# Optimization experiments

Hardware: AMD Instinct MI355X
Metric: run time of the kernel (lower is better)

Reference implementation:

```python
import jax, jax.numpy as jnp
import numpy as np

B, K, PS, DP = 8, 8, 128, 16           # batch, patches/example, patch px, dino patch size
D, NH, HD, L = 1024, 8, 128, 2         # embed dim, heads, head dim, transformer layers
GRID = PS // DP                        # 8 tokens per side
TPP = GRID * GRID                      # 64 tokens per patch


def _conv(x, w, stride, pad):
    return jax.lax.conv_general_dilated(x, w, (stride, stride), pad,
                                        dimension_numbers=('NCHW', 'OIHW', 'NCHW'))


def _ln(x, g, b, eps=1e-5):
    m = jnp.mean(x, -1, keepdims=True)
    v = jnp.var(x, -1, keepdims=True)
    return (x - m) * jax.lax.rsqrt(v + eps) * g + b


def _bn(x, g, b, m, v, eps=1e-5):
    inv = jax.lax.rsqrt(v + eps)
    return (x - m[:, None, None]) * inv[:, None, None] * g[:, None, None] + b[:, None, None]


def _up2(x):  # bilinear x2, align_corners=False (half-pixel, matches jax.image.resize)
    n, c, h, w = x.shape
    return jax.image.resize(x, (n, c, 2 * h, 2 * w), method='linear')


def _mha(x, wqkv, bqkv, wo, bo):
    b, s, d = x.shape
    qkv = x @ wqkv.T + bqkv
    q, k, v = jnp.split(qkv, 3, axis=-1)
    q = q.reshape(b, s, NH, HD).transpose(0, 2, 1, 3)
    k = k.reshape(b, s, NH, HD).transpose(0, 2, 1, 3)
    v = v.reshape(b, s, NH, HD).transpose(0, 2, 1, 3)
    att = jax.nn.softmax(jnp.einsum('bhqd,bhkd->bhqk', q, k) / jnp.sqrt(jnp.float32(HD)), axis=-1)
    o = jnp.einsum('bhqk,bhkd->bhqd', att, v).transpose(0, 2, 1, 3).reshape(b, s, d)
    return o @ wo.T + bo


def setup_inputs() -> dict:
    key = jax.random.key(0)
    ks = iter(jax.random.split(key, 40))

    def rn(shape, s=0.02):
        return jax.random.normal(next(ks), shape, jnp.float32) * s

    inp = {}
    inp['patches'] = jax.random.normal(next(ks), (B, K, 3, PS, PS), jnp.float32)
    inp['pe_w'] = rn((D, 3, DP, DP))
    inp['pe_b'] = jnp.zeros((D,), jnp.float32)
    inp['qkv_w'] = rn((L, 3 * D, D))
    inp['qkv_b'] = jnp.zeros((L, 3 * D), jnp.float32)
    inp['out_w'] = rn((L, D, D))
    inp['out_b'] = jnp.zeros((L, D), jnp.float32)
    inp['ln1_g'] = jnp.ones((L, D), jnp.float32)
    inp['ln1_b'] = jnp.zeros((L, D), jnp.float32)
    inp['ff1_w'] = rn((L, 4 * D, D))
    inp['ff1_b'] = jnp.zeros((L, 4 * D), jnp.float32)
    inp['ff2_w'] = rn((L, D, 4 * D))
    inp['ff2_b'] = jnp.zeros((L, D), jnp.float32)
    inp['ln2_g'] = jnp.ones((L, D), jnp.float32)
    inp['ln2_b'] = jnp.zeros((L, D), jnp.float32)
    chans = [(512, D), (256, 512), (128, 256), (64, 128)]
    for i, (co, ci) in enumerate(chans, 1):
        inp[f'dw{i}'] = rn((co, ci, 3, 3), 0.05)
        inp[f'db{i}'] = jnp.zeros((co,), jnp.float32)
        inp[f'g{i}'] = jnp.ones((co,), jnp.float32)
        inp[f'be{i}'] = jnp.zeros((co,), jnp.float32)
        inp[f'm{i}'] = jnp.zeros((co,), jnp.float32)
        inp[f'v{i}'] = jnp.ones((co,), jnp.float32)
    inp['dw5'] = rn((1, 64, 1, 1), 0.05)
    inp['db5'] = jnp.zeros((1,), jnp.float32)
    return inp


def reference(patches, pe_w, pe_b, qkv_w, qkv_b, out_w, out_b, ln1_g, ln1_b,
              ff1_w, ff1_b, ff2_w, ff2_b, ln2_g, ln2_b,
              dw1, db1, g1, be1, m1, v1, dw2, db2, g2, be2, m2, v2,
              dw3, db3, g3, be3, m3, v3, dw4, db4, g4, be4, m4, v4, dw5, db5):
    b, k = patches.shape[:2]
    x = patches.reshape(b * k, 3, PS, PS)
    # frozen DINO patch embedding (runs under torch.no_grad in the original)
    hs = _conv(x, pe_w, DP, 'VALID') + pe_b[None, :, None, None]     # [BK, D, GRID, GRID]
    hs = jax.lax.stop_gradient(hs)
    hs = hs.reshape(b * k, D, TPP).transpose(0, 2, 1).reshape(b, k * TPP, D)
    # post-norm TransformerEncoder (norm_first=False, gelu), dropout=eval (identity)
    for i in range(L):
        hs = _ln(hs + _mha(hs, qkv_w[i], qkv_b[i], out_w[i], out_b[i]), ln1_g[i], ln1_b[i])
        ff = jax.nn.gelu(hs @ ff1_w[i].T + ff1_b[i], approximate=False) @ ff2_w[i].T + ff2_b[i]
        hs = _ln(hs + ff, ln2_g[i], ln2_b[i])
    fm = hs.reshape(b * k, TPP, D).transpose(0, 2, 1).reshape(b * k, D, GRID, GRID)
    # CNN decoder: (conv3x3 -> BN(eval) -> ReLU -> bilinear x2) x4 -> conv1x1
    y = _up2(jax.nn.relu(_bn(_conv(fm, dw1, 1, 'SAME') + db1[None, :, None, None], g1, be1, m1, v1)))
    y = _up2(jax.nn.relu(_bn(_conv(y, dw2, 1, 'SAME') + db2[None, :, None, None], g2, be2, m2, v2)))
    y = _up2(jax.nn.relu(_bn(_conv(y, dw3, 1, 'SAME') + db3[None, :, None, None], g3, be3, m3, v3)))
    y = _up2(jax.nn.relu(_bn(_conv(y, dw4, 1, 'SAME') + db4[None, :, None, None], g4, be4, m4, v4)))
    y = _conv(y, dw5, 1, 'VALID') + db5[None, :, None, None]          # [BK, 1, PS, PS]
    return y.reshape(b, k, 1, PS, PS)
```

## Files before the change

### kernel.cpp

```cpp
#include <hip/hip_runtime.h>
#include <stdint.h>


typedef unsigned short u16;
typedef __bf16 bf16x8 __attribute__((ext_vector_type(8)));
typedef short  s16x8  __attribute__((ext_vector_type(8)));
typedef float  f32x4  __attribute__((ext_vector_type(4)));

__device__ __forceinline__ float b2f(u16 x) { return __uint_as_float(((unsigned)x) << 16); }
__device__ __forceinline__ u16 f2b(float f) {
  unsigned u = __float_as_uint(f);
  unsigned r = (u + 0x7fffu + ((u >> 16) & 1u)) >> 16;
  return (u16)r;
}
__device__ __forceinline__ void async16(u16* lds, const u16* g) {
  __builtin_amdgcn_global_load_lds((const __attribute__((address_space(1))) void*)g,
                                   (__attribute__((address_space(3))) void*)lds, 16, 0, 0);
}
__device__ __forceinline__ float gelu_f(float x) {
  return 0.5f * x * (1.0f + erff(x * 0.70710678118654752f));
}

__global__ __launch_bounds__(256) void cvt_f2b(const float* __restrict__ src,
                                               u16* __restrict__ dst, int n) {
  const int i = (blockIdx.x * 256 + threadIdx.x) * 4;
  if (i + 3 < n) {
    const float4 v = *(const float4*)(src + i);
    dst[i] = f2b(v.x); dst[i + 1] = f2b(v.y); dst[i + 2] = f2b(v.z); dst[i + 3] = f2b(v.w);
  }
}

__global__ __launch_bounds__(256) void gemm_bt(
    const u16* __restrict__ A, int lda, long long sAb, long long sAh,
    const u16* __restrict__ B, int ldb, long long sBb, long long sBh,
    u16* __restrict__ Cb, int ldc, long long sCb, long long sCh,
    const float* __restrict__ bias, int epi, int ZH, int nk)
{
  __shared__ u16 As[3][128 * 32];
  __shared__ u16 Bs[3][128 * 32];
  const int tid = threadIdx.x;
  const int zb = blockIdx.z / ZH, zh = blockIdx.z % ZH;
  const u16* Ab = A + zb * sAb + zh * sAh;
  const u16* Bb = B + zb * sBb + zh * sBh;
  const int m0 = blockIdx.y << 7, n0 = blockIdx.x << 7;
  const int wave = tid >> 6, lane = tid & 63;
  const int wm = (wave >> 1) << 6, wn = (wave & 1) << 6;
  const int lr = lane & 15, lq = lane >> 4;
  const int rowb = tid >> 2;
  const int kc_e = (((tid & 3) ^ ((tid >> 3) & 3)) << 3);
  const int kslot = ((lq ^ ((lr >> 1) & 3)) << 3);

  const u16* Arow0 = Ab + (long long)(m0 + rowb)      * lda + kc_e;
  const u16* Arow1 = Ab + (long long)(m0 + rowb + 64) * lda + kc_e;
  const u16* Brow0 = Bb + (long long)(n0 + rowb)      * ldb + kc_e;
  const u16* Brow1 = Bb + (long long)(n0 + rowb + 64) * ldb + kc_e;

  f32x4 acc[4][4] = {};

  auto stage = [&](int kt, int b) {
    const int k0 = kt << 5;
    async16(&As[b][tid * 8],         Arow0 + k0);
    async16(&As[b][(tid + 256) * 8], Arow1 + k0);
    async16(&Bs[b][tid * 8],         Brow0 + k0);
    async16(&Bs[b][(tid + 256) * 8], Brow1 + k0);
  };

  stage(0, 0);
  if (nk > 1) stage(1, 1);
  int cur = 0;
  for (int kt = 0; kt < nk; ++kt) {
    if (kt + 2 < nk) {
      int nb = cur + 2; if (nb >= 3) nb -= 3;
      stage(kt + 2, nb);
      asm volatile("s_waitcnt vmcnt(8)" ::: "memory");
    } else if (kt + 1 < nk) {
      asm volatile("s_waitcnt vmcnt(4)" ::: "memory");
    } else {
      asm volatile("s_waitcnt vmcnt(0)" ::: "memory");
    }
    asm volatile("s_barrier" ::: "memory");

    bf16x8 af[4], bfv[4];
#pragma unroll
    for (int mi = 0; mi < 4; ++mi)
      af[mi] = __builtin_bit_cast(bf16x8, *(const s16x8*)&As[cur][((wm + mi * 16 + lr) << 5) + kslot]);
#pragma unroll
    for (int ni = 0; ni < 4; ++ni)
      bfv[ni] = __builtin_bit_cast(bf16x8, *(const s16x8*)&Bs[cur][((wn + ni * 16 + lr) << 5) + kslot]);
#pragma unroll
    for (int mi = 0; mi < 4; ++mi)
#pragma unroll
      for (int ni = 0; ni < 4; ++ni)
        acc[mi][ni] = __builtin_amdgcn_mfma_f32_16x16x32_bf16(af[mi], bfv[ni], acc[mi][ni], 0, 0, 0);

    asm volatile("s_barrier" ::: "memory");
    ++cur; if (cur == 3) cur = 0;
  }

  const long long Co = zb * sCb + zh * sCh;
#pragma unroll
  for (int ni = 0; ni < 4; ++ni) {
    const int col = n0 + wn + ni * 16 + lr;
    const float badd = bias ? bias[col] : 0.0f;
#pragma unroll
    for (int mi = 0; mi < 4; ++mi) {
      const int row0 = m0 + wm + mi * 16 + (lq << 2);
#pragma unroll
      for (int r = 0; r < 4; ++r) {
        float v = acc[mi][ni][r] + badd;
        if (epi == 1) v = gelu_f(v);
        Cb[Co + (long long)(row0 + r) * ldc + col] = f2b(v);
      }
    }
  }
}

__global__ __launch_bounds__(256) void conv_gemm(
    const u16* __restrict__ U, const u16* __restrict__ Wr,
    u16* __restrict__ Out,
    const float* __restrict__ bn_g, const float* __restrict__ bn_b,
    const float* __restrict__ bn_m, const float* __restrict__ bn_v,
    const float* __restrict__ cb,
    const u16* __restrict__ zpg,
    int H, int W, int l2w, int l2hw, int l2c, int CoutReal, int Kdim, int nk)
{
  __shared__ u16 As[3][128 * 32];
  __shared__ u16 Bs[3][64 * 32];
  const int tid = threadIdx.x;
  const int m0 = blockIdx.x << 7, n0 = blockIdx.y << 6;
  const int wave = tid >> 6, lane = tid & 63;
  const int wm = (wave >> 1) << 6, wn = (wave & 1) << 5;
  const int lr = lane & 15, lq = lane >> 4;
  const int rowb = tid >> 2;
  const int kc_e = (((tid & 3) ^ ((tid >> 3) & 3)) << 3);
  const int kslot = ((lq ^ ((lr >> 1) & 3)) << 3);
  const int hwmask = (1 << l2hw) - 1, wmask = (1 << l2w) - 1, cmask = (1 << l2c) - 1;

  int yA[2], xA[2];
  long long baseA[2];
  {
#pragma unroll
    for (int i = 0; i < 2; ++i) {
      const int mrow = m0 + rowb + (i << 6);
      const int img = mrow >> l2hw;
      const int rem = mrow & hwmask;
      yA[i] = rem >> l2w; xA[i] = rem & wmask;
      baseA[i] = (long long)(img << l2hw);
    }
  }
  const u16* Bbase = Wr + (long long)(n0 + rowb) * Kdim + kc_e;

  f32x4 acc[4][2] = {};

  auto stage = [&](int kt, int b) {
    const int k0 = kt << 5;
    const int k = k0 + kc_e;
    const int t = k >> l2c, ci = k & cmask;
    const int dy = (t * 86) >> 8;
    const int dx = t - dy * 3;
#pragma unroll
    for (int i = 0; i < 2; ++i) {
      const int yy = yA[i] + dy - 1, xx = xA[i] + dx - 1;
      const u16* src = ((unsigned)yy < (unsigned)H && (unsigned)xx < (unsigned)W)
          ? U + (((baseA[i] + (yy << l2w) + xx) << l2c) + ci)
          : zpg;
      async16(&As[b][(tid + (i << 8)) * 8], src);
    }
    async16(&Bs[b][tid * 8], Bbase + k0);
  };

  stage(0, 0);
  stage(1, 1);

  for (int t0 = 0; t0 < nk; t0 += 3) {
#pragma unroll
    for (int p = 0; p < 3; ++p) {
      const int tt = t0 + p;
      if (tt + 2 < nk) {
        stage(tt + 2, (p + 2) % 3);
        asm volatile("s_waitcnt vmcnt(6)" ::: "memory");
      } else if (tt + 1 < nk) {
        asm volatile("s_waitcnt vmcnt(3)" ::: "memory");
      } else {
        asm volatile("s_waitcnt vmcnt(0)" ::: "memory");
      }
      asm volatile("s_barrier" ::: "memory");

      bf16x8 af[4], bfv[2];
#pragma unroll
      for (int mi = 0; mi < 4; ++mi)
        af[mi] = __builtin_bit_cast(bf16x8, *(const s16x8*)&As[p][((wm + mi * 16 + lr) << 5) + kslot]);
#pragma unroll
      for (int ni = 0; ni < 2; ++ni)
        bfv[ni] = __builtin_bit_cast(bf16x8, *(const s16x8*)&Bs[p][((wn + ni * 16 + lr) << 5) + kslot]);
#pragma unroll
      for (int mi = 0; mi < 4; ++mi)
#pragma unroll
        for (int ni = 0; ni < 2; ++ni)
          acc[mi][ni] = __builtin_amdgcn_mfma_f32_16x16x32_bf16(af[mi], bfv[ni], acc[mi][ni], 0, 0, 0);

      asm volatile("s_barrier" ::: "memory");
    }
  }

#pragma unroll
  for (int ni = 0; ni < 2; ++ni) {
    const int col = n0 + wn + ni * 16 + lr;
    const bool ok = col < CoutReal;
    float bs = 0.0f, bsh = 0.0f;
    if (ok) {
      const float inv = rsqrtf(bn_v[col] + 1e-5f);
      bs = bn_g[col] * inv;
      bsh = (cb[col] - bn_m[col]) * bs + bn_b[col];
    }
#pragma unroll
    for (int mi = 0; mi < 4; ++mi) {
      const int row0 = m0 + wm + mi * 16 + (lq << 2);
#pragma unroll
      for (int r = 0; r < 4; ++r) {
        if (ok) {
          const float v = fmaxf(acc[mi][ni][r] * bs + bsh, 0.0f);
          Out[(long long)(row0 + r) * CoutReal + col] = f2b(v);
        }
      }
    }
  }
}


__global__ void pe_gather(const float* __restrict__ patches, u16* __restrict__ Ape) {
  const int t = blockIdx.x, tid = threadIdx.x;
  const int img = t >> 6, pos = t & 63, ty = pos >> 3, tx = pos & 7;
  const float* base = patches + (long long)img * 3 * 128 * 128;
  u16* dst = Ape + (long long)t * 768;
  for (int k = tid; k < 768; k += 256) {
    const int c = k >> 8, rr = k & 255, ky = rr >> 4, kx = rr & 15;
    dst[k] = f2b(base[c * 16384 + (ty * 16 + ky) * 128 + tx * 16 + kx]);
  }
}

__global__ void vt_transpose(const u16* __restrict__ qkv, u16* __restrict__ Vt) {
  __shared__ u16 lds[64 * 130];
  const int tt = blockIdx.x;
  const int z = blockIdx.y;
  const int bq = z >> 3, h = z & 7;
  const int tid = threadIdx.x;
  for (int idx = tid; idx < 64 * 128; idx += 256) {
    const int t = idx >> 7, d = idx & 127;
    lds[t * 130 + d] = qkv[(long long)(bq * 512 + tt * 64 + t) * 3072 + 2048 + h * 128 + d];
  }
  __syncthreads();
  for (int idx = tid; idx < 64 * 128; idx += 256) {
    const int d = idx >> 6, t = idx & 63;
    Vt[(long long)z * 65536 + d * 512 + tt * 64 + t] = lds[t * 130 + d];
  }
}

__global__ __launch_bounds__(256) void softmax_rows(u16* __restrict__ P) {
  __shared__ float red[8];
  const long long base = (long long)blockIdx.x * 512;
  const int tid = threadIdx.x;
  const float sc = 0.08838834764831845f;
  float x0 = b2f(P[base + tid]) * sc;
  float x1 = b2f(P[base + tid + 256]) * sc;
  float mx = fmaxf(x0, x1);
  for (int o = 32; o; o >>= 1) mx = fmaxf(mx, __shfl_down(mx, o));
  if ((tid & 63) == 0) red[tid >> 6] = mx;
  __syncthreads();
  mx = fmaxf(fmaxf(red[0], red[1]), fmaxf(red[2], red[3]));
  const float e0 = expf(x0 - mx), e1 = expf(x1 - mx);
  float s = e0 + e1;
  for (int o = 32; o; o >>= 1) s += __shfl_down(s, o);
  __syncthreads();
  if ((tid & 63) == 0) red[tid >> 6] = s;
  __syncthreads();
  s = red[0] + red[1] + red[2] + red[3];
  const float inv = 1.0f / s;
  P[base + tid] = f2b(e0 * inv);
  P[base + tid + 256] = f2b(e1 * inv);
}

__global__ __launch_bounds__(256) void ln_kernel(
    u16* __restrict__ hsb, const u16* __restrict__ P,
    const float* __restrict__ gw, const float* __restrict__ bw)
{
  __shared__ float red[8];
  const int r = blockIdx.x, tid = threadIdx.x;
  float x[4], s = 0.0f, s2 = 0.0f;
#pragma unroll
  for (int i = 0; i < 4; ++i) {
    const int c = tid + i * 256;
    const float v = b2f(hsb[(long long)r * 1024 + c]) + b2f(P[(long long)r * 1024 + c]);
    x[i] = v; s += v; s2 += v * v;
  }
  for (int o = 32; o; o >>= 1) { s += __shfl_down(s, o); s2 += __shfl_down(s2, o); }
  if ((tid & 63) == 0) { red[tid >> 6] = s; red[4 + (tid >> 6)] = s2; }
  __syncthreads();
  s  = red[0] + red[1] + red[2] + red[3];
  s2 = red[4] + red[5] + red[6] + red[7];
  const float mean = s * (1.0f / 1024.0f);
  const float var = s2 * (1.0f / 1024.0f) - mean * mean;
  const float inv = rsqrtf(var + 1e-5f);
#pragma unroll
  for (int i = 0; i < 4; ++i) {
    const int c = tid + i * 256;
    const float y = (x[i] - mean) * inv * gw[c] + bw[c];
    hsb[(long long)r * 1024 + c] = f2b(y);
  }
}

__global__ void repack_w(const float* __restrict__ src, u16* __restrict__ dst, int Cout, int l2c) {
  const int co = blockIdx.x, tid = threadIdx.x;
  const int Cin = 1 << l2c, K9 = 9 << l2c;
  for (int j = tid; j < K9; j += 256) {
    const int t = j >> l2c, ci = j & (Cin - 1);
    u16 v = 0;
    if (co < Cout) v = f2b(src[(long long)(co * Cin + ci) * 9 + t]);
    dst[(long long)co * K9 + j] = v;
  }
}

__global__ void ups2x(const u16* __restrict__ in, u16* __restrict__ out,
                      int l2h, int l2w, int l2c, long long total)
{
  const long long idx = (long long)blockIdx.x * 256 + threadIdx.x;
  if (idx >= total) return;
  const int H = 1 << l2h, W = 1 << l2w, C = 1 << l2c;
  const int c = (int)(idx & (C - 1));
  long long t = idx >> l2c;
  const int ox = (int)(t & (2 * W - 1)); t >>= (l2w + 1);
  const int oy = (int)(t & (2 * H - 1)); t >>= (l2h + 1);
  const int img = (int)t;
  const int iy = oy >> 1, ix = ox >> 1;
  int y0, y1, x0, x1; float wy0, wy1, wx0, wx1;
  if (oy & 1) { y0 = iy; y1 = min(iy + 1, H - 1); wy0 = 0.75f; wy1 = 0.25f; }
  else        { y0 = max(iy - 1, 0); y1 = iy;     wy0 = 0.25f; wy1 = 0.75f; }
  if (ox & 1) { x0 = ix; x1 = min(ix + 1, W - 1); wx0 = 0.75f; wx1 = 0.25f; }
  else        { x0 = max(ix - 1, 0); x1 = ix;     wx0 = 0.25f; wx1 = 0.75f; }
  const u16* base = in + (((long long)img) << (l2h + l2w + l2c));
  const float v00 = b2f(base[((((long long)y0 << l2w) + x0) << l2c) + c]);
  const float v01 = b2f(base[((((long long)y0 << l2w) + x1) << l2c) + c]);
  const float v10 = b2f(base[((((long long)y1 << l2w) + x0) << l2c) + c]);
  const float v11 = b2f(base[((((long long)y1 << l2w) + x1) << l2c) + c]);
  out[idx] = f2b(wy0 * (wx0 * v00 + wx1 * v01) + wy1 * (wx0 * v10 + wx1 * v11));
}

__global__ __launch_bounds__(256) void conv1x1_final(
    const u16* __restrict__ C4, const float* __restrict__ w5,
    const float* __restrict__ b5, float* __restrict__ Z)
{
  const int tid = threadIdx.x;
  const int px = blockIdx.x * 4 + (tid >> 6);
  const int lane = tid & 63;
  float v = b2f(C4[(long long)px * 64 + lane]) * w5[lane];
  for (int o = 32; o; o >>= 1) v += __shfl_down(v, o);
  if (lane == 0) Z[px] = v + b5[0];
}

__global__ void ups_final(const float* __restrict__ Z, float* __restrict__ out) {
  const int idx = blockIdx.x * 256 + threadIdx.x;
  const int ox = idx & 127, oy = (idx >> 7) & 127, img = idx >> 14;
  const int iy = oy >> 1, ix = ox >> 1;
  int y0, y1, x0, x1; float wy0, wy1, wx0, wx1;
  if (oy & 1) { y0 = iy; y1 = min(iy + 1, 63); wy0 = 0.75f; wy1 = 0.25f; }
  else        { y0 = max(iy - 1, 0); y1 = iy;  wy0 = 0.25f; wy1 = 0.75f; }
  if (ox & 1) { x0 = ix; x1 = min(ix + 1, 63); wx0 = 0.75f; wx1 = 0.25f; }
  else        { x0 = max(ix - 1, 0); x1 = ix;  wx0 = 0.25f; wx1 = 0.75f; }
  const float* zi = Z + (long long)img * 4096;
  const float v = wy0 * (wx0 * zi[y0 * 64 + x0] + wx1 * zi[y0 * 64 + x1]) +
                  wy1 * (wx0 * zi[y1 * 64 + x0] + wx1 * zi[y1 * 64 + x1]);
  out[idx] = v;
}

extern "C" void kernel_launch(void* const* d_in, const int* in_sizes, int n_in,
                              void* d_out, int out_size, void* d_ws, size_t ws_size,
                              hipStream_t stream)
{
  (void)in_sizes; (void)n_in; (void)out_size;
  if (ws_size < 110395648u) return;
  const float* patches = (const float*)d_in[0];
  const float* pe_w = (const float*)d_in[1];
  const float* pe_b = (const float*)d_in[2];
  const float* qkv_w = (const float*)d_in[3];
  const float* qkv_b = (const float*)d_in[4];
  const float* out_w = (const float*)d_in[5];
  const float* out_b = (const float*)d_in[6];
  const float* ln1_g = (const float*)d_in[7];
  const float* ln1_b = (const float*)d_in[8];
  const float* ff1_w = (const float*)d_in[9];
  const float* ff1_b = (const float*)d_in[10];
  const float* ff2_w = (const float*)d_in[11];
  const float* ff2_b = (const float*)d_in[12];
  const float* ln2_g = (const float*)d_in[13];
  const float* ln2_b = (const float*)d_in[14];
  const float* dwv[4] = {(const float*)d_in[15], (const float*)d_in[21], (const float*)d_in[27], (const float*)d_in[33]};
  const float* dbv[4] = {(const float*)d_in[16], (const float*)d_in[22], (const float*)d_in[28], (const float*)d_in[34]};
  const float* gv[4]  = {(const float*)d_in[17], (const float*)d_in[23], (const float*)d_in[29], (const float*)d_in[35]};
  const float* bev[4] = {(const float*)d_in[18], (const float*)d_in[24], (const float*)d_in[30], (const float*)d_in[36]};
  const float* mv[4]  = {(const float*)d_in[19], (const float*)d_in[25], (const float*)d_in[31], (const float*)d_in[37]};
  const float* vv[4]  = {(const float*)d_in[20], (const float*)d_in[26], (const float*)d_in[32], (const float*)d_in[38]};
  const float* dw5 = (const float*)d_in[39];
  const float* db5 = (const float*)d_in[40];
  float* outp = (float*)d_out;
  char* ws = (char*)d_ws;

  u16* HS_B = (u16*)(ws + 0);
  u16* APE  = (u16*)(ws + 8388608);
  u16* QKV  = (u16*)(ws + 8388608);
  u16* VT   = (u16*)(ws + 33554432);
  u16* SF   = (u16*)(ws + 41943040);
  u16* FF1G = (u16*)(ws + 41943040);
  u16* ATT  = (u16*)(ws + 75497472);
  u16* P_B  = (u16*)(ws + 83886080);
  u16* W1   = (u16*)(ws + 92274688);
  u16* W2   = (u16*)(ws + 100663296);
  u16* WR1 = (u16*)(ws + 8388608);
  u16* WR2 = (u16*)(ws + 17825792);
  u16* WR3 = (u16*)(ws + 20185088);
  u16* C1  = (u16*)(ws + 20774912);
  u16* U1  = (u16*)(ws + 24969216);
  u16* C2  = (u16*)(ws + 41746432);
  u16* U2  = (u16*)(ws + 50135040);
  u16* C3  = (u16*)(ws + 83689472);
  u16* U3  = (u16*)(ws + 8388608);
  u16* C4  = (u16*)(ws + 75497472);
  u16* ZPG = (u16*)(ws + 109051904);
  u16* WR4 = (u16*)(ws + 109052160);
  float* Z = (float*)(ws + 109347072);

  pe_gather<<<4096, 256, 0, stream>>>(patches, APE);
  cvt_f2b<<<768, 256, 0, stream>>>(pe_w, W1, 786432);
  gemm_bt<<<dim3(8, 32, 1), 256, 0, stream>>>(
      APE, 768, 0, 0, W1, 768, 0, 0,
      HS_B, 1024, 0, 0, pe_b, 0, 1, 24);

  for (int l = 0; l < 2; ++l) {
    cvt_f2b<<<3072, 256, 0, stream>>>(qkv_w + (long long)l * 3145728, W1, 3145728);
    gemm_bt<<<dim3(24, 32, 1), 256, 0, stream>>>(
        HS_B, 1024, 0, 0, W1, 1024, 0, 0,
        QKV, 3072, 0, 0, qkv_b + l * 3072, 0, 1, 32);
    vt_transpose<<<dim3(8, 64), 256, 0, stream>>>(QKV, VT);
    gemm_bt<<<dim3(4, 4, 64), 256, 0, stream>>>(
        QKV, 3072, 1572864, 128, QKV + 1024, 3072, 1572864, 128,
        SF, 512, 2097152, 262144, nullptr, 0, 8, 4);
    softmax_rows<<<32768, 256, 0, stream>>>(SF);
    gemm_bt<<<dim3(1, 4, 64), 256, 0, stream>>>(
        SF, 512, 2097152, 262144, VT, 512, 524288, 65536,
        ATT, 1024, 524288, 128, nullptr, 0, 8, 16);
    cvt_f2b<<<1024, 256, 0, stream>>>(out_w + (long long)l * 1048576, W2, 1048576);
    gemm_bt<<<dim3(8, 32, 1), 256, 0, stream>>>(
        ATT, 1024, 0, 0, W2, 1024, 0, 0,
        P_B, 1024, 0, 0, out_b + l * 1024, 0, 1, 32);
    ln_kernel<<<4096, 256, 0, stream>>>(HS_B, P_B, ln1_g + l * 1024, ln1_b + l * 1024);
    cvt_f2b<<<4096, 256, 0, stream>>>(ff1_w + (long long)l * 4194304, W1, 4194304);
    cvt_f2b<<<4096, 256, 0, stream>>>(ff2_w + (long long)l * 4194304, W2, 4194304);
    gemm_bt<<<dim3(32, 32, 1), 256, 0, stream>>>(
        HS_B, 1024, 0, 0, W1, 1024, 0, 0,
        FF1G, 4096, 0, 0, ff1_b + l * 4096, 1, 1, 32);
    gemm_bt<<<dim3(8, 32, 1), 256, 0, stream>>>(
        FF1G, 4096, 0, 0, W2, 4096, 0, 0,
        P_B, 1024, 0, 0, ff2_b + l * 1024, 0, 1, 128);
    ln_kernel<<<4096, 256, 0, stream>>>(HS_B, P_B, ln2_g + l * 1024, ln2_b + l * 1024);
  }

  hipMemsetAsync((void*)ZPG, 0, 256, stream);
  repack_w<<<512, 256, 0, stream>>>(dwv[0], WR1, 512, 10);
  repack_w<<<256, 256, 0, stream>>>(dwv[1], WR2, 256, 9);
  repack_w<<<128, 256, 0, stream>>>(dwv[2], WR3, 128, 8);
  repack_w<<<128, 256, 0, stream>>>(dwv[3], WR4, 64, 7);

  conv_gemm<<<dim3(32, 8, 1), 256, 0, stream>>>(
      HS_B, WR1, C1, gv[0], bev[0], mv[0], vv[0], dbv[0], ZPG,
      8, 8, 3, 6, 10, 512, 9216, 288);
  ups2x<<<32768, 256, 0, stream>>>(C1, U1, 3, 3, 9, 8388608LL);
  conv_gemm<<<dim3(128, 4, 1), 256, 0, stream>>>(
      U1, WR2, C2, gv[1], bev[1], mv[1], vv[1], dbv[1], ZPG,
      16, 16, 4, 8, 9, 256, 4608, 144);
  ups2x<<<65536, 256, 0, stream>>>(C2, U2, 4, 4, 8, 16777216LL);
  conv_gemm<<<dim3(512, 2, 1), 256, 0, stream>>>(
      U2, WR3, C3, gv[2], bev[2], mv[2], vv[2], dbv[2], ZPG,
      32, 32, 5, 10, 8, 128, 2304, 72);
  ups2x<<<131072, 256, 0, stream>>>(C3, U3, 5, 5, 7, 33554432LL);
  conv_gemm<<<dim3(2048, 1, 1), 256, 0, stream>>>(
      U3, WR4, C4, gv[3], bev[3], mv[3], vv[3], dbv[3], ZPG,
      64, 64, 6, 12, 7, 64, 1152, 36);
  conv1x1_final<<<65536, 256, 0, stream>>>(C4, dw5, db5, Z);
  ups_final<<<4096, 256, 0, stream>>>(Z, outp);
}
```

Measured before the change: 1.396 ms.

## Split-K low-occupancy GEMMs and early convs with fp32 partial reduction kernels

After: 1.306 ms. 6.5% less time.

```diff
diff --git a/kernel.cpp b/kernel.cpp
--- a/kernel.cpp
+++ b/kernel.cpp
@@ -34,7 +34,8 @@
     const u16* __restrict__ A, int lda, long long sAb, long long sAh,
     const u16* __restrict__ B, int ldb, long long sBb, long long sBh,
     u16* __restrict__ Cb, int ldc, long long sCb, long long sCh,
-    const float* __restrict__ bias, int epi, int ZH, int nk)
+    const float* __restrict__ bias, int epi, int ZH, int nk,
+    float* __restrict__ Part)
 {
   __shared__ u16 As[3][128 * 32];
   __shared__ u16 Bs[3][128 * 32];
@@ -47,13 +48,14 @@
   const int wm = (wave >> 1) << 6, wn = (wave & 1) << 6;
   const int lr = lane & 15, lq = lane >> 4;
   const int rowb = tid >> 2;
+  const int koff = Part ? (zb * (nk << 5)) : 0;
   const int kc_e = (((tid & 3) ^ ((tid >> 3) & 3)) << 3);
   const int kslot = ((lq ^ ((lr >> 1) & 3)) << 3);
 
-  const u16* Arow0 = Ab + (long long)(m0 + rowb)      * lda + kc_e;
-  const u16* Arow1 = Ab + (long long)(m0 + rowb + 64) * lda + kc_e;
-  const u16* Brow0 = Bb + (long long)(n0 + rowb)      * ldb + kc_e;
-  const u16* Brow1 = Bb + (long long)(n0 + rowb + 64) * ldb + kc_e;
+  const u16* Arow0 = Ab + (long long)(m0 + rowb)      * lda + kc_e + koff;
+  const u16* Arow1 = Ab + (long long)(m0 + rowb + 64) * lda + kc_e + koff;
+  const u16* Brow0 = Bb + (long long)(n0 + rowb)      * ldb + kc_e + koff;
+  const u16* Brow1 = Bb + (long long)(n0 + rowb + 64) * ldb + kc_e + koff;
 
   f32x4 acc[4][4] = {};
 
@@ -97,6 +99,22 @@
     ++cur; if (cur == 3) cur = 0;
   }
 
+  if (Part) {
+    float* P = Part + (long long)zb * sCb;
+#pragma unroll
+    for (int ni = 0; ni < 4; ++ni) {
+      const int col = n0 + wn + ni * 16 + lr;
+#pragma unroll
+      for (int mi = 0; mi < 4; ++mi) {
+        const int row0 = m0 + wm + mi * 16 + (lq << 2);
+#pragma unroll
+        for (int r = 0; r < 4; ++r)
+          P[(long long)(row0 + r) * ldc + col] = acc[mi][ni][r];
+      }
+    }
+    return;
+  }
+
   const long long Co = zb * sCb + zh * sCh;
 #pragma unroll
   for (int ni = 0; ni < 4; ++ni) {
@@ -112,6 +130,49 @@
         Cb[Co + (long long)(row0 + r) * ldc + col] = f2b(v);
       }
     }
+  }
+}
+
+__global__ __launch_bounds__(256) void reduce_bias(
+    const float* __restrict__ Part, long long sPart, int S,
+    const float* __restrict__ bias, int N,
+    u16* __restrict__ Out, long long total)
+{
+  const long long i = ((long long)blockIdx.x * 256 + threadIdx.x) * 4;
+  if (i >= total) return;
+  f32x4 s = *(const f32x4*)(Part + i);
+  for (int p = 1; p < S; ++p) {
+    const f32x4 v = *(const f32x4*)(Part + (long long)p * sPart + i);
+    s[0] += v[0]; s[1] += v[1]; s[2] += v[2]; s[3] += v[3];
+  }
+  const int colb = (int)(i & (N - 1));
+#pragma unroll
+  for (int j = 0; j < 4; ++j)
+    Out[i + j] = f2b(s[j] + bias[colb + j]);
+}
+
+__global__ __launch_bounds__(256) void reduce_bn(
+    const float* __restrict__ Part, long long sPart, int S,
+    const float* __restrict__ bn_g, const float* __restrict__ bn_b,
+    const float* __restrict__ bn_m, const float* __restrict__ bn_v,
+    const float* __restrict__ cb, int Cout,
+    u16* __restrict__ Out, long long total)
+{
+  const long long i = ((long long)blockIdx.x * 256 + threadIdx.x) * 4;
+  if (i >= total) return;
+  f32x4 s = *(const f32x4*)(Part + i);
+  for (int p = 1; p < S; ++p) {
+    const f32x4 v = *(const f32x4*)(Part + (long long)p * sPart + i);
+    s[0] += v[0]; s[1] += v[1]; s[2] += v[2]; s[3] += v[3];
+  }
+  const int colb = (int)(i & (Cout - 1));
+#pragma unroll
+  for (int j = 0; j < 4; ++j) {
+    const int col = colb + j;
+    const float inv = rsqrtf(bn_v[col] + 1e-5f);
+    const float bs = bn_g[col] * inv;
+    const float bsh = (cb[col] - bn_m[col]) * bs + bn_b[col];
+    Out[i + j] = f2b(fmaxf(s[j] * bs + bsh, 0.0f));
   }
 }
 
@@ -122,12 +183,15 @@
     const float* __restrict__ bn_m, const float* __restrict__ bn_v,
     const float* __restrict__ cb,
     const u16* __restrict__ zpg,
-    int H, int W, int l2w, int l2hw, int l2c, int CoutReal, int Kdim, int nk)
+    int H, int W, int l2w, int l2hw, int l2c, int CoutReal, int Kdim, int nk,
+    float* __restrict__ Part, long long sPart)
 {
   __shared__ u16 As[3][128 * 32];
   __shared__ u16 Bs[3][64 * 32];
   const int tid = threadIdx.x;
   const int m0 = blockIdx.x << 7, n0 = blockIdx.y << 6;
+  const int slice = blockIdx.z;
+  const int koff = Part ? (slice * (nk << 5)) : 0;
   const int wave = tid >> 6, lane = tid & 63;
   const int wm = (wave >> 1) << 6, wn = (wave & 1) << 5;
   const int lr = lane & 15, lq = lane >> 4;
@@ -148,14 +212,14 @@
       baseA[i] = (long long)(img << l2hw);
     }
   }
-  const u16* Bbase = Wr + (long long)(n0 + rowb) * Kdim + kc_e;
+  const u16* Bbase = Wr + (long long)(n0 + rowb) * Kdim + kc_e + koff;
 
   f32x4 acc[4][2] = {};
 
   auto stage = [&](int kt, int b) {
     const int k0 = kt << 5;
-    const int k = k0 + kc_e;
-    const int t = k >> l2c, ci = k & cmask;
+    const int kabs = koff + k0 + kc_e;
+    const int t = kabs >> l2c, ci = kabs & cmask;
     const int dy = (t * 86) >> 8;
     const int dx = t - dy * 3;
 #pragma unroll
@@ -201,6 +265,22 @@
 
       asm volatile("s_barrier" ::: "memory");
     }
+  }
+
+  if (Part) {
+    float* P = Part + (long long)slice * sPart;
+#pragma unroll
+    for (int ni = 0; ni < 2; ++ni) {
+      const int col = n0 + wn + ni * 16 + lr;
+#pragma unroll
+      for (int mi = 0; mi < 4; ++mi) {
+        const int row0 = m0 + wm + mi * 16 + (lq << 2);
+#pragma unroll
+        for (int r = 0; r < 4; ++r)
+          P[(long long)(row0 + r) * CoutReal + col] = acc[mi][ni][r];
+      }
+    }
+    return;
   }
 
 #pragma unroll
@@ -414,6 +494,8 @@
   u16* P_B  = (u16*)(ws + 83886080);
   u16* W1   = (u16*)(ws + 92274688);
   u16* W2   = (u16*)(ws + 100663296);
+  float* PART_G  = (float*)(ws + 8388608);
+  float* PART_PE = (float*)(ws + 41943040);
   u16* WR1 = (u16*)(ws + 8388608);
   u16* WR2 = (u16*)(ws + 17825792);
   u16* WR3 = (u16*)(ws + 20185088);
@@ -424,42 +506,47 @@
   u16* C3  = (u16*)(ws + 83689472);
   u16* U3  = (u16*)(ws + 8388608);
   u16* C4  = (u16*)(ws + 75497472);
+  float* PARTC1 = (float*)(ws + 41746432);
+  float* PARTC2 = (float*)(ws + 50331648);
   u16* ZPG = (u16*)(ws + 109051904);
   u16* WR4 = (u16*)(ws + 109052160);
   float* Z = (float*)(ws + 109347072);
 
   pe_gather<<<4096, 256, 0, stream>>>(patches, APE);
   cvt_f2b<<<768, 256, 0, stream>>>(pe_w, W1, 786432);
-  gemm_bt<<<dim3(8, 32, 1), 256, 0, stream>>>(
+  gemm_bt<<<dim3(8, 32, 2), 256, 0, stream>>>(
       APE, 768, 0, 0, W1, 768, 0, 0,
-      HS_B, 1024, 0, 0, pe_b, 0, 1, 24);
+      HS_B, 1024, 4194304, 0, nullptr, 0, 1, 12, PART_PE);
+  reduce_bias<<<4096, 256, 0, stream>>>(PART_PE, 4194304, 2, pe_b, 1024, HS_B, 4194304LL);
 
   for (int l = 0; l < 2; ++l) {
     cvt_f2b<<<3072, 256, 0, stream>>>(qkv_w + (long long)l * 3145728, W1, 3145728);
     gemm_bt<<<dim3(24, 32, 1), 256, 0, stream>>>(
         HS_B, 1024, 0, 0, W1, 1024, 0, 0,
-        QKV, 3072, 0, 0, qkv_b + l * 3072, 0, 1, 32);
+        QKV, 3072, 0, 0, qkv_b + l * 3072, 0, 1, 32, nullptr);
     vt_transpose<<<dim3(8, 64), 256, 0, stream>>>(QKV, VT);
     gemm_bt<<<dim3(4, 4, 64), 256, 0, stream>>>(
         QKV, 3072, 1572864, 128, QKV + 1024, 3072, 1572864, 128,
-        SF, 512, 2097152, 262144, nullptr, 0, 8, 4);
+        SF, 512, 2097152, 262144, nullptr, 0, 8, 4, nullptr);
     softmax_rows<<<32768, 256, 0, stream>>>(SF);
     gemm_bt<<<dim3(1, 4, 64), 256, 0, stream>>>(
         SF, 512, 2097152, 262144, VT, 512, 524288, 65536,
-        ATT, 1024, 524288, 128, nullptr, 0, 8, 16);
+        ATT, 1024, 524288, 128, nullptr, 0, 8, 16, nullptr);
     cvt_f2b<<<1024, 256, 0, stream>>>(out_w + (long long)l * 1048576, W2, 1048576);
-    gemm_bt<<<dim3(8, 32, 1), 256, 0, stream>>>(
+    gemm_bt<<<dim3(8, 32, 2), 256, 0, stream>>>(
         ATT, 1024, 0, 0, W2, 1024, 0, 0,
-        P_B, 1024, 0, 0, out_b + l * 1024, 0, 1, 32);
+        P_B, 1024, 4194304, 0, nullptr, 0, 1, 16, PART_G);
+    reduce_bias<<<4096, 256, 0, stream>>>(PART_G, 4194304, 2, out_b + l * 1024, 1024, P_B, 4194304LL);
     ln_kernel<<<4096, 256, 0, stream>>>(HS_B, P_B, ln1_g + l * 1024, ln1_b + l * 1024);
     cvt_f2b<<<4096, 256, 0, stream>>>(ff1_w + (long long)l * 4194304, W1, 4194304);
     cvt_f2b<<<4096, 256, 0, stream>>>(ff2_w + (long long)l * 4194304, W2, 4194304);
     gemm_bt<<<dim3(32, 32, 1), 256, 0, stream>>>(
         HS_B, 1024, 0, 0, W1, 1024, 0, 0,
-        FF1G, 4096, 0, 0, ff1_b + l * 4096, 1, 1, 32);
-    gemm_bt<<<dim3(8, 32, 1), 256, 0, stream>>>(
+        FF1G, 4096, 0, 0, ff1_b + l * 4096, 1, 1, 32, nullptr);
+    gemm_bt<<<dim3(8, 32, 2), 256, 0, stream>>>(
         FF1G, 4096, 0, 0, W2, 4096, 0, 0,
-        P_B, 1024, 0, 0, ff2_b + l * 1024, 0, 1, 128);
+        P_B, 1024, 4194304, 0, nullptr, 0, 1, 64, PART_G);
+    reduce_bias<<<4096, 256, 0, stream>>>(PART_G, 4194304, 2, ff2_b + l * 1024, 1024, P_B, 4194304LL);
     ln_kernel<<<4096, 256, 0, stream>>>(HS_B, P_B, ln2_g + l * 1024, ln2_b + l * 1024);
   }
 
@@ -469,21 +556,25 @@
   repack_w<<<128, 256, 0, stream>>>(dwv[2], WR3, 128, 8);
   repack_w<<<128, 256, 0, stream>>>(dwv[3], WR4, 64, 7);
 
-  conv_gemm<<<dim3(32, 8, 1), 256, 0, stream>>>(
+  conv_gemm<<<dim3(32, 8, 4), 256, 0, stream>>>(
       HS_B, WR1, C1, gv[0], bev[0], mv[0], vv[0], dbv[0], ZPG,
-      8, 8, 3, 6, 10, 512, 9216, 288);
+      8, 8, 3, 6, 10, 512, 9216, 72, PARTC1, 2097152);
+  reduce_bn<<<2048, 256, 0, stream>>>(PARTC1, 2097152, 4,
+      gv[0], bev[0], mv[0], vv[0], dbv[0], 512, C1, 2097152LL);
   ups2x<<<32768, 256, 0, stream>>>(C1, U1, 3, 3, 9, 8388608LL);
-  conv_gemm<<<dim3(128, 4, 1), 256, 0, stream>>>(
+  conv_gemm<<<dim3(128, 4, 2), 256, 0, stream>>>(
       U1, WR2, C2, gv[1], bev[1], mv[1], vv[1], dbv[1], ZPG,
-      16, 16, 4, 8, 9, 256, 4608, 144);
+      16, 16, 4, 8, 9, 256, 4608, 72, PARTC2, 4194304);
+  reduce_bn<<<4096, 256, 0, stream>>>(PARTC2, 4194304, 2,
+      gv[1], bev[1], mv[1], vv[1], dbv[1], 256, C2, 4194304LL);
   ups2x<<<65536, 256, 0, stream>>>(C2, U2, 4, 4, 8, 16777216LL);
   conv_gemm<<<dim3(512, 2, 1), 256, 0, stream>>>(
       U2, WR3, C3, gv[2], bev[2], mv[2], vv[2], dbv[2], ZPG,
-      32, 32, 5, 10, 8, 128, 2304, 72);
+      32, 32, 5, 10, 8, 128, 2304, 72, nullptr, 0);
   ups2x<<<131072, 256, 0, stream>>>(C3, U3, 5, 5, 7, 33554432LL);
   conv_gemm<<<dim3(2048, 1, 1), 256, 0, stream>>>(
       U3, WR4, C4, gv[3], bev[3], mv[3], vv[3], dbv[3], ZPG,
-      64, 64, 6, 12, 7, 64, 1152, 36);
+      64, 64, 6, 12, 7, 64, 1152, 36, nullptr, 0);
   conv1x1_final<<<65536, 256, 0, stream>>>(C4, dw5, db5, Z);
   ups_final<<<4096, 256, 0, stream>>>(Z, outp);
 }
```
